# Optimization experiments

Measured on AMD Instinct MI355X. Metric: run time of the kernel, lower is better.

Reference implementation:

```python
import jax, jax.numpy as jnp
import numpy as np

B, T, H = 512, 256, 1024


def setup_inputs() -> dict:
    key = jax.random.key(0)
    ks = jax.random.split(key, 7)
    s = 1.0 / np.sqrt(H)
    return {
        "x": jax.random.normal(ks[0], (B, T), dtype=jnp.float32),
        "W_ih": jax.random.normal(ks[1], (4 * H, 1), dtype=jnp.float32) * s,
        "W_hh": jax.random.normal(ks[2], (4 * H, H), dtype=jnp.float32) * s,
        "b_ih": jax.random.normal(ks[3], (4 * H,), dtype=jnp.float32) * s,
        "b_hh": jax.random.normal(ks[4], (4 * H,), dtype=jnp.float32) * s,
        "W_out": jax.random.normal(ks[5], (1, H), dtype=jnp.float32) * s,
        "b_out": jax.random.normal(ks[6], (1,), dtype=jnp.float32) * s,
    }


def reference(x, W_ih, W_hh, b_ih, b_hh, W_out, b_out):
    # x: [B, T]; LSTMCell recurrence over T with a linear head per step.
    Bx, Tx = x.shape
    Hh = W_hh.shape[1]
    b = b_ih + b_hh  # [4H]
    xs = x.T[:, :, None]  # [T, B, 1] timestep slices

    def step(carry, x_t):
        h, c = carry
        # gates: [B, 4H] = x_t @ W_ih^T + h @ W_hh^T + b (torch LSTMCell order i,f,g,o)
        gates = x_t @ W_ih.T + h @ W_hh.T + b
        i, f, g, o = jnp.split(gates, 4, axis=-1)
        i = jax.nn.sigmoid(i)
        f = jax.nn.sigmoid(f)
        g = jnp.tanh(g)
        o = jax.nn.sigmoid(o)
        c = f * c + i * g
        h = o * jnp.tanh(c)
        out = h @ W_out.T + b_out  # [B, 1]
        return (h, c), out

    h0 = jnp.zeros((Bx, Hh), dtype=x.dtype)
    c0 = jnp.zeros((Bx, Hh), dtype=x.dtype)
    _, outs = jax.lax.scan(step, (h0, c0), xs)  # outs: [T, B, 1]
    # torch.stack(outputs, 1).squeeze(2) -> [B, T]
    return outs[:, :, 0].T
```

## Files before the change

kernel.cpp:

```cpp
#include <hip/hip_runtime.h>
#include <hip/hip_fp16.h>
#include <hip/hip_cooperative_groups.h>

#define B_ 512
#define T_ 256
#define H_ 1024
#define G4_ 4096
#define KL_ 20
#define KR_ 8
#define KS_ 4

typedef _Float16 half8 __attribute__((ext_vector_type(8)));
typedef float f32x4 __attribute__((ext_vector_type(4)));

__device__ __forceinline__ float fast_sigmoid(float x) {
    return 1.0f / (1.0f + __expf(-x));
}
__device__ __forceinline__ float fast_tanh(float x) {
    float x2 = fminf(fmaxf(2.0f * x, -30.0f), 30.0f);
    float e = __expf(x2);
    return (e - 1.0f) / (e + 1.0f);
}

__global__ void pack_w(const float* __restrict__ Whh,
                       _Float16* __restrict__ Wlds, _Float16* __restrict__ Wl2) {
    int idx = blockIdx.x * blockDim.x + threadIdx.x;
    int gc = idx >> 10, k = idx & 1023;
    int nt = gc >> 10, u = gc & 1023;
    int jb = u >> 4, lk = u & 15;
    int ki = k >> 5, hi = (k >> 3) & 3, e = k & 7;
    int l = hi * 16 + lk;
    _Float16 v = (_Float16)Whh[idx];
    int frag = nt * 512 + l * 8 + e;
    if (ki < KL_) {
        int slot = jb >> 1, wj = jb & 1;
        Wlds[(size_t)slot * 81920 + wj * 40960 + ki * 2048 + frag] = v;
    } else {
        Wl2[(size_t)jb * 24576 + (ki - KL_) * 2048 + frag] = v;
    }
}

__global__ void init_misc(const float* __restrict__ bih, const float* __restrict__ bhh,
                          const float* __restrict__ bout,
                          float* __restrict__ bias, float* __restrict__ out) {
    int idx = blockIdx.x * blockDim.x + threadIdx.x;
    if (idx < G4_) bias[idx] = bih[idx] + bhh[idx];
    if (idx < B_ * T_) out[idx] = bout[0];
}

__global__ __launch_bounds__(512, 1)
void lstm_persist(const _Float16* __restrict__ Wlds,
                  const _Float16* __restrict__ Wl2,
                  const float* __restrict__ bias,
                  const float* __restrict__ x,
                  const float* __restrict__ Wih,
                  const float* __restrict__ Wout,
                  _Float16* __restrict__ hbuf,
                  float* __restrict__ out,
                  unsigned int* __restrict__ cnts) {
    extern __shared__ _Float16 Wl[];
    cooperative_groups::grid_group grid = cooperative_groups::this_grid();

    const int tid = threadIdx.x;
    unsigned int xcc;
    asm volatile("s_getreg_b32 %0, hwreg(HW_REG_XCC_ID)" : "=s"(xcc));
    const int xcd = (int)(xcc & 7u);
    if (tid == 0) {
        unsigned int s = __hip_atomic_fetch_add(&cnts[xcd], 1u,
                                                __ATOMIC_RELAXED, __HIP_MEMORY_SCOPE_AGENT);
        __hip_atomic_store(&cnts[512 + blockIdx.x], s,
                           __ATOMIC_RELAXED, __HIP_MEMORY_SCOPE_AGENT);
    }
    grid.sync();
    const int slot = (int)__hip_atomic_load(&cnts[512 + blockIdx.x],
                                            __ATOMIC_RELAXED, __HIP_MEMORY_SCOPE_AGENT);
    const int nactive = (int)min(32u, __hip_atomic_load(&cnts[xcd], __ATOMIC_RELAXED,
                                                        __HIP_MEMORY_SCOPE_AGENT));
    if (slot >= 32) return;

    const int w = tid >> 6, l = tid & 63;
    const int lk = l & 15, hi = l >> 4;
    const int wr = w >> 1, wj = w & 1;
    const int row0 = wr * 16;
    const int u = slot * 32 + wj * 16 + lk;

    {
        const half8* src = (const half8*)(Wlds + (size_t)slot * 81920);
        half8* dst = (half8*)Wl;
#pragma unroll
        for (int o = 0; o < 20; ++o) dst[tid + o * 512] = src[tid + o * 512];
    }
    const _Float16* Bg = Wl2 + ((size_t)slot * 2 + wj) * 24576 + l * 8;
    half8 breg[KR_ * 4];
#pragma unroll
    for (int kg = 0; kg < KR_; ++kg)
#pragma unroll
        for (int nt = 0; nt < 4; ++nt)
            breg[kg * 4 + nt] = *(const half8*)(Bg + kg * 2048 + nt * 512);
#pragma unroll
    for (int q = 0; q < KR_ * 4; ++q) asm volatile("" : "+v"(breg[q]));

    float bz[4], wi4[4];
#pragma unroll
    for (int nt = 0; nt < 4; ++nt) {
        int gc = nt * 1024 + u;
        bz[nt] = bias[gc];
        wi4[nt] = Wih[gc];
    }
    const float wout = Wout[u];
    int rowsl[4], rowsg[4];
#pragma unroll
    for (int r = 0; r < 4; ++r) {
        rowsl[r] = row0 + hi * 4 + r;
        rowsg[r] = xcd * 64 + rowsl[r];
    }
    const int kb = u >> 3, ue = u & 7;
    f32x4 creg = {0.f, 0.f, 0.f, 0.f};
    __syncthreads();

    _Float16* hx = hbuf + (size_t)xcd * 2 * 65536;
    const _Float16* Bgs = Bg + KR_ * 2048;
    unsigned int* barp = &cnts[16 + xcd * 32];

    float xv[4];
#pragma unroll
    for (int r = 0; r < 4; ++r) xv[r] = x[rowsg[r] * T_];

    for (int t = 0; t < T_; ++t) {
        if (t > 0) {
            if (tid == 0) {
                unsigned int tgt = (unsigned int)nactive * (unsigned int)t;
                while (__hip_atomic_load(barp, __ATOMIC_RELAXED, __HIP_MEMORY_SCOPE_AGENT) < tgt)
                    __builtin_amdgcn_s_sleep(2);
            }
            __syncthreads();
            asm volatile("buffer_inv sc0" ::: "memory");
        }

        const int wb = t & 1, rb = wb ^ 1;
        f32x4 acc[4];
#pragma unroll
        for (int nt = 0; nt < 4; ++nt) {
#pragma unroll
            for (int r = 0; r < 4; ++r) acc[nt][r] = bz[nt] + xv[r] * wi4[nt];
        }

        if (t > 0) {
            const _Float16* Ap = hx + rb * 65536 + hi * 512 + (row0 + lk) * 8;
            half8 bs[8];
#pragma unroll
            for (int q = 0; q < 8; ++q)
                bs[q] = *(const half8*)(Bgs + (q >> 2) * 2048 + (q & 3) * 512);
#pragma unroll
            for (int ki = 0; ki < 10; ++ki) {
                half8 a = *(const half8*)(Ap + ki * 2048);
                const _Float16* bp = Wl + wj * 40960 + ki * 2048 + l * 8;
#pragma unroll
                for (int nt = 0; nt < 4; ++nt) {
                    half8 b = *(const half8*)(bp + nt * 512);
                    acc[nt] = __builtin_amdgcn_mfma_f32_16x16x32_f16(a, b, acc[nt], 0, 0, 0);
                }
            }
            half8 bs2[8];
#pragma unroll
            for (int q = 0; q < 8; ++q)
                bs2[q] = *(const half8*)(Bgs + (2 + (q >> 2)) * 2048 + (q & 3) * 512);
#pragma unroll
            for (int ki = 10; ki < KL_; ++ki) {
                half8 a = *(const half8*)(Ap + ki * 2048);
                const _Float16* bp = Wl + wj * 40960 + ki * 2048 + l * 8;
#pragma unroll
                for (int nt = 0; nt < 4; ++nt) {
                    half8 b = *(const half8*)(bp + nt * 512);
                    acc[nt] = __builtin_amdgcn_mfma_f32_16x16x32_f16(a, b, acc[nt], 0, 0, 0);
                }
            }
#pragma unroll
            for (int kg = 0; kg < KR_; ++kg) {
                half8 a = *(const half8*)(Ap + (KL_ + kg) * 2048);
#pragma unroll
                for (int nt = 0; nt < 4; ++nt)
                    acc[nt] = __builtin_amdgcn_mfma_f32_16x16x32_f16(a, breg[kg * 4 + nt], acc[nt], 0, 0, 0);
            }
#pragma unroll
            for (int kg = 0; kg < 2; ++kg) {
                half8 a = *(const half8*)(Ap + (KL_ + KR_ + kg) * 2048);
#pragma unroll
                for (int nt = 0; nt < 4; ++nt)
                    acc[nt] = __builtin_amdgcn_mfma_f32_16x16x32_f16(a, bs[kg * 4 + nt], acc[nt], 0, 0, 0);
            }
#pragma unroll
            for (int kg = 0; kg < 2; ++kg) {
                half8 a = *(const half8*)(Ap + (KL_ + KR_ + 2 + kg) * 2048);
#pragma unroll
                for (int nt = 0; nt < 4; ++nt)
                    acc[nt] = __builtin_amdgcn_mfma_f32_16x16x32_f16(a, bs2[kg * 4 + nt], acc[nt], 0, 0, 0);
            }
        }

        _Float16* hn = hx + wb * 65536;
        float p4[4];
#pragma unroll
        for (int r = 0; r < 4; ++r) {
            float iv = fast_sigmoid(acc[0][r]);
            float fv = fast_sigmoid(acc[1][r]);
            float gv = fast_tanh(acc[2][r]);
            float ov = fast_sigmoid(acc[3][r]);
            float cv = fv * creg[r] + iv * gv;
            creg[r] = cv;
            float hv = ov * fast_tanh(cv);
            hn[(kb * 64 + rowsl[r]) * 8 + ue] = (_Float16)hv;
            p4[r] = hv * wout;
        }

        if (t < T_ - 1) {
            __syncthreads();
            if (tid == 0)
                __hip_atomic_fetch_add(barp, 1u, __ATOMIC_RELAXED, __HIP_MEMORY_SCOPE_AGENT);
        }

#pragma unroll
        for (int m = 1; m <= 8; m <<= 1) {
#pragma unroll
            for (int r = 0; r < 4; ++r) p4[r] += __shfl_xor(p4[r], m);
        }
        if (lk == 0) {
#pragma unroll
            for (int r = 0; r < 4; ++r)
                atomicAdd(&out[rowsg[r] * T_ + t], p4[r]);
        }
        if (t < T_ - 1) {
#pragma unroll
            for (int r = 0; r < 4; ++r) xv[r] = x[rowsg[r] * T_ + t + 1];
        }
    }
}

extern "C" void kernel_launch(void* const* d_in, const int* in_sizes, int n_in,
                              void* d_out, int out_size, void* d_ws, size_t ws_size,
                              hipStream_t stream) {
    const float* x    = (const float*)d_in[0];
    const float* Wih  = (const float*)d_in[1];
    const float* Whh  = (const float*)d_in[2];
    const float* bih  = (const float*)d_in[3];
    const float* bhh  = (const float*)d_in[4];
    const float* Wout = (const float*)d_in[5];
    const float* bout = (const float*)d_in[6];
    float* out = (float*)d_out;

    char* ws = (char*)d_ws;
    _Float16* Wlds = (_Float16*)ws;
    _Float16* Wl2  = (_Float16*)(ws + 5242880);
    _Float16* hbuf = (_Float16*)(ws + (8 << 20));
    float* bias    = (float*)(ws + (10 << 20));
    unsigned int* cnts = (unsigned int*)(ws + (10 << 20) + (64 << 10));

    hipMemsetAsync(cnts, 0, 4096, stream);
    pack_w<<<(G4_ * H_) / 256, 256, 0, stream>>>(Whh, Wlds, Wl2);
    init_misc<<<512, 256, 0, stream>>>(bih, bhh, bout, bias, out);

    (void)hipFuncSetAttribute((const void*)lstm_persist,
                              hipFuncAttributeMaxDynamicSharedMemorySize, 163840);
    void* args[] = {&Wlds, &Wl2, &bias, &x, &Wih, &Wout, &hbuf, &out, &cnts};
    hipLaunchCooperativeKernel((void*)lstm_persist, dim3(256), dim3(512),
                               args, 163840, stream);
}
```

Measured before the change: 1.791 ms.

## Replace cooperative launch and cache invalidate with atomic barrier and atomic h loads

Swaps the cooperative launch and grid.sync for a normal launch plus a hand-written atomic counter barrier at startup. Drops the per-step buffer_inv cache invalidation and instead reads the shared hidden state through relaxed agent-scope 64-bit atomic loads, which bypass stale cache lines. The aim is to cut cooperative-launch overhead and the cost of invalidating the whole cache each timestep. The risk is that splitting each 128-bit load into two atomic 64-bit loads may cost more per load, and that the spin barrier assumes all 256 blocks are co-resident, which is no longer guaranteed without a cooperative launch.

```diff
diff --git a/kernel.cpp b/kernel.cpp
--- a/kernel.cpp
+++ b/kernel.cpp
@@ -1,6 +1,5 @@
 #include <hip/hip_runtime.h>
 #include <hip/hip_fp16.h>
-#include <hip/hip_cooperative_groups.h>
 
 #define B_ 512
 #define T_ 256
@@ -12,6 +11,7 @@
 
 typedef _Float16 half8 __attribute__((ext_vector_type(8)));
 typedef float f32x4 __attribute__((ext_vector_type(4)));
+typedef unsigned long long u64;
 
 __device__ __forceinline__ float fast_sigmoid(float x) {
     return 1.0f / (1.0f + __expf(-x));
@@ -20,6 +20,14 @@
     float x2 = fminf(fmaxf(2.0f * x, -30.0f), 30.0f);
     float e = __expf(x2);
     return (e - 1.0f) / (e + 1.0f);
+}
+
+__device__ __forceinline__ half8 loadA(const _Float16* p) {
+    union { half8 h; u64 q[2]; } v;
+    const u64* q = (const u64*)p;
+    v.q[0] = __hip_atomic_load(q,     __ATOMIC_RELAXED, __HIP_MEMORY_SCOPE_AGENT);
+    v.q[1] = __hip_atomic_load(q + 1, __ATOMIC_RELAXED, __HIP_MEMORY_SCOPE_AGENT);
+    return v.h;
 }
 
 __global__ void pack_w(const float* __restrict__ Whh,
@@ -59,7 +67,6 @@
                   float* __restrict__ out,
                   unsigned int* __restrict__ cnts) {
     extern __shared__ _Float16 Wl[];
-    cooperative_groups::grid_group grid = cooperative_groups::this_grid();
 
     const int tid = threadIdx.x;
     unsigned int xcc;
@@ -70,8 +77,11 @@
                                                 __ATOMIC_RELAXED, __HIP_MEMORY_SCOPE_AGENT);
         __hip_atomic_store(&cnts[512 + blockIdx.x], s,
                            __ATOMIC_RELAXED, __HIP_MEMORY_SCOPE_AGENT);
-    }
-    grid.sync();
+        __hip_atomic_fetch_add(&cnts[8], 1u, __ATOMIC_ACQ_REL, __HIP_MEMORY_SCOPE_AGENT);
+        while (__hip_atomic_load(&cnts[8], __ATOMIC_ACQUIRE, __HIP_MEMORY_SCOPE_AGENT) < 256u)
+            __builtin_amdgcn_s_sleep(2);
+    }
+    __syncthreads();
     const int slot = (int)__hip_atomic_load(&cnts[512 + blockIdx.x],
                                             __ATOMIC_RELAXED, __HIP_MEMORY_SCOPE_AGENT);
     const int nactive = (int)min(32u, __hip_atomic_load(&cnts[xcd], __ATOMIC_RELAXED,
@@ -134,7 +144,6 @@
                     __builtin_amdgcn_s_sleep(2);
             }
             __syncthreads();
-            asm volatile("buffer_inv sc0" ::: "memory");
         }
 
         const int wb = t & 1, rb = wb ^ 1;
@@ -153,7 +162,7 @@
                 bs[q] = *(const half8*)(Bgs + (q >> 2) * 2048 + (q & 3) * 512);
 #pragma unroll
             for (int ki = 0; ki < 10; ++ki) {
-                half8 a = *(const half8*)(Ap + ki * 2048);
+                half8 a = loadA(Ap + ki * 2048);
                 const _Float16* bp = Wl + wj * 40960 + ki * 2048 + l * 8;
 #pragma unroll
                 for (int nt = 0; nt < 4; ++nt) {
@@ -167,7 +176,7 @@
                 bs2[q] = *(const half8*)(Bgs + (2 + (q >> 2)) * 2048 + (q & 3) * 512);
 #pragma unroll
             for (int ki = 10; ki < KL_; ++ki) {
-                half8 a = *(const half8*)(Ap + ki * 2048);
+                half8 a = loadA(Ap + ki * 2048);
                 const _Float16* bp = Wl + wj * 40960 + ki * 2048 + l * 8;
 #pragma unroll
                 for (int nt = 0; nt < 4; ++nt) {
@@ -177,21 +186,21 @@
             }
 #pragma unroll
             for (int kg = 0; kg < KR_; ++kg) {
-                half8 a = *(const half8*)(Ap + (KL_ + kg) * 2048);
+                half8 a = loadA(Ap + (KL_ + kg) * 2048);
 #pragma unroll
                 for (int nt = 0; nt < 4; ++nt)
                     acc[nt] = __builtin_amdgcn_mfma_f32_16x16x32_f16(a, breg[kg * 4 + nt], acc[nt], 0, 0, 0);
             }
 #pragma unroll
             for (int kg = 0; kg < 2; ++kg) {
-                half8 a = *(const half8*)(Ap + (KL_ + KR_ + kg) * 2048);
+                half8 a = loadA(Ap + (KL_ + KR_ + kg) * 2048);
 #pragma unroll
                 for (int nt = 0; nt < 4; ++nt)
                     acc[nt] = __builtin_amdgcn_mfma_f32_16x16x32_f16(a, bs[kg * 4 + nt], acc[nt], 0, 0, 0);
             }
 #pragma unroll
             for (int kg = 0; kg < 2; ++kg) {
-                half8 a = *(const half8*)(Ap + (KL_ + KR_ + 2 + kg) * 2048);
+                half8 a = loadA(Ap + (KL_ + KR_ + 2 + kg) * 2048);
 #pragma unroll
                 for (int nt = 0; nt < 4; ++nt)
                     acc[nt] = __builtin_amdgcn_mfma_f32_16x16x32_f16(a, bs2[kg * 4 + nt], acc[nt], 0, 0, 0);
@@ -261,7 +270,6 @@
 
     (void)hipFuncSetAttribute((const void*)lstm_persist,
                               hipFuncAttributeMaxDynamicSharedMemorySize, 163840);
-    void* args[] = {&Wlds, &Wl2, &bias, &x, &Wih, &Wout, &hbuf, &out, &cnts};
-    hipLaunchCooperativeKernel((void*)lstm_persist, dim3(256), dim3(512),
-                               args, 163840, stream);
-}
+    lstm_persist<<<dim3(256), dim3(512), 163840, stream>>>(
+        Wlds, Wl2, bias, x, Wih, Wout, hbuf, out, cnts);
+}
```

Measured after the change: 4.825 ms. 169% more time.
